# Kernel tuning notes

Measured on AMD Instinct MI355X. Metric: run time of the kernel, lower is better.

Reference implementation:

```python
import jax, jax.numpy as jnp
import numpy as np

D_MODEL = 32
NHEAD = 4
NUM_LAYERS = 4
WINDOW = 256
D_FF = 2 * D_MODEL
INPUT_DIM = 58
MAX_DEPTH = 12
HEAD_OUT = 25


def _layernorm(x, g, b, eps=1e-5):
    m = jnp.mean(x, axis=-1, keepdims=True)
    v = jnp.mean((x - m) ** 2, axis=-1, keepdims=True)
    return (x - m) / jnp.sqrt(v + eps) * g + b


def _layer(h, ipw, ipb, opw, opb, g1, b1, w1, bb1, w2, bb2, g2, b2):
    # Post-norm transformer layer (subclass overrides parent's norm_first path).
    Wn, S, D = h.shape
    dh = D // NHEAD
    qkv = h @ ipw.T + ipb                      # [Wn, S, 3D]
    q, k, v = jnp.split(qkv, 3, axis=-1)
    q = q.reshape(Wn, S, NHEAD, dh).transpose(0, 2, 1, 3)  # [Wn,H,S,dh]
    k = k.reshape(Wn, S, NHEAD, dh).transpose(0, 2, 1, 3)
    v = v.reshape(Wn, S, NHEAD, dh).transpose(0, 2, 1, 3)
    scores = jnp.einsum('whqd,whkd->whqk', q, k) / jnp.sqrt(jnp.asarray(dh, h.dtype))
    a = jax.nn.softmax(scores, axis=-1)        # eager attn weights (need_weights=True path)
    o = jnp.einsum('whqk,whkd->whqd', a, v).transpose(0, 2, 1, 3).reshape(Wn, S, D)
    o = o @ opw.T + opb
    h = _layernorm(h + o, g1, b1)
    ff = jax.nn.gelu(h @ w1.T + bb1, approximate=False) @ w2.T + bb2
    return _layernorm(h + ff, g2, b2)


def setup_inputs() -> dict:
    key = jax.random.key(0)
    ks = jax.random.split(key, 24)
    B, N = 2, 65536
    x = jax.random.uniform(ks[0], (B, N, INPUT_DIM), dtype=jnp.float32)
    layers = jax.random.randint(ks[1], (B, N), 0, MAX_DEPTH)

    def w(k, shape, s=0.05):
        return jax.random.normal(k, shape, jnp.float32) * s

    L = NUM_LAYERS
    return dict(
        x=x,
        layers=layers,
        feature_proj_w=w(ks[2], (D_MODEL, INPUT_DIM)),
        feature_proj_b=w(ks[3], (D_MODEL,)),
        layer_embed=w(ks[4], (MAX_DEPTH, D_MODEL)),
        fourier_B=jax.random.normal(ks[5], (3, D_MODEL // 2), jnp.float32) * 1024.0,
        in_proj_w=w(ks[6], (L, 3 * D_MODEL, D_MODEL)),
        in_proj_b=w(ks[7], (L, 3 * D_MODEL)),
        out_proj_w=w(ks[8], (L, D_MODEL, D_MODEL)),
        out_proj_b=w(ks[9], (L, D_MODEL)),
        ln1_g=jnp.ones((L, D_MODEL), jnp.float32),
        ln1_b=jnp.zeros((L, D_MODEL), jnp.float32),
        lin1_w=w(ks[10], (L, D_FF, D_MODEL)),
        lin1_b=w(ks[11], (L, D_FF)),
        lin2_w=w(ks[12], (L, D_MODEL, D_FF)),
        lin2_b=w(ks[13], (L, D_MODEL)),
        ln2_g=jnp.ones((L, D_MODEL), jnp.float32),
        ln2_b=jnp.zeros((L, D_MODEL), jnp.float32),
        norm_out_g=jnp.ones((D_MODEL,), jnp.float32),
        norm_out_b=jnp.zeros((D_MODEL,), jnp.float32),
        head_w=w(ks[14], (HEAD_OUT, D_MODEL)),
        head_b=w(ks[15], (HEAD_OUT,)),
    )


def reference(x, layers, feature_proj_w, feature_proj_b, layer_embed, fourier_B,
              in_proj_w, in_proj_b, out_proj_w, out_proj_b,
              ln1_g, ln1_b, lin1_w, lin1_b, lin2_w, lin2_b, ln2_g, ln2_b,
              norm_out_g, norm_out_b, head_w, head_b):
    B, N, _ = x.shape
    pos = x[:, :, :3]
    proj = (2.0 * jnp.pi) * (pos @ fourier_B)                  # [B,N,D/2]
    pe = jnp.concatenate([jnp.sin(proj), jnp.cos(proj)], axis=-1)
    h = x @ feature_proj_w.T + feature_proj_b + layer_embed[layers] + pe
    # N chosen divisible by WINDOW, so pad_len == 0 (original pads otherwise)
    nw = N // WINDOW
    h = h.reshape(B * nw, WINDOW, D_MODEL)
    for i in range(NUM_LAYERS):
        h = _layer(h, in_proj_w[i], in_proj_b[i], out_proj_w[i], out_proj_b[i],
                   ln1_g[i], ln1_b[i], lin1_w[i], lin1_b[i], lin2_w[i], lin2_b[i],
                   ln2_g[i], ln2_b[i])
    h = h.reshape(B, N, D_MODEL)
    return _layernorm(h, norm_out_g, norm_out_b) @ head_w.T + head_b
```

## Files before the change

kernel.cpp:

```cpp
#include <hip/hip_runtime.h>

constexpr int S    = 256;
constexpr int D    = 32;
constexpr int NH   = 4;
constexpr int DH   = 8;
constexpr int DFF  = 64;
constexpr int NL   = 4;
constexpr int IND  = 58;
constexpr int HOUT = 25;
constexpr int TPB  = 256;

typedef float  f2 __attribute__((ext_vector_type(2)));
typedef float  f4 __attribute__((ext_vector_type(4)));
typedef __fp16 h2 __attribute__((ext_vector_type(2)));
typedef __fp16 h4 __attribute__((ext_vector_type(4)));
typedef __fp16 h8 __attribute__((ext_vector_type(8)));

__device__ __forceinline__ f4 MFMA16(h4 a, h4 b, f4 c) {
  return __builtin_amdgcn_mfma_f32_16x16x16f16(a, b, c, 0, 0, 0);
}
__device__ __forceinline__ f4 MFMA32(h8 a, h8 b, f4 c) {
  return __builtin_amdgcn_mfma_f32_16x16x32_f16(a, b, c, 0, 0, 0);
}
__device__ __forceinline__ h8 hcat(h4 a, h4 b) {
  return __builtin_shufflevector(a, b, 0, 1, 2, 3, 4, 5, 6, 7);
}

constexpr int HOFF  = 0;
constexpr int QKOFF = 16384;
constexpr int VOFF  = 49152;

__device__ __forceinline__ unsigned pk2(float a, float b) {
  h2 h = __builtin_amdgcn_cvt_pkrtz(a, b);
  return __builtin_bit_cast(unsigned, h);
}

__device__ __forceinline__ float exp2fast(float x) {
#if __has_builtin(__builtin_amdgcn_exp2f)
  return __builtin_amdgcn_exp2f(x);
#else
  return exp2f(x);
#endif
}

__device__ __forceinline__ void wave_fence() {
  __builtin_amdgcn_wave_barrier();
  __builtin_amdgcn_sched_barrier(0);
}

template<int NF2>
__device__ __forceinline__ float dotp(const float* __restrict__ w,
                                      const float* __restrict__ v) {
  const f2* W = (const f2*)w;
  const f2* V = (const f2*)v;
  f2 a0 = {0.f, 0.f}, a1 = {0.f, 0.f};
#pragma unroll
  for (int i = 0; i < NF2; i += 2) a0 += V[i] * W[i];
#pragma unroll
  for (int i = 1; i < NF2; i += 2) a1 += V[i] * W[i];
  f2 s = a0 + a1;
  return s.x + s.y;
}

__device__ __forceinline__ float gelu(float x) {
  float u = 2.3022082f * fmaf(0.044715f * x * x, x, x);
  return x * __builtin_amdgcn_rcpf(1.0f + exp2fast(-u));
}

__device__ __forceinline__ void lnorm(float* h, const float* __restrict__ g,
                                      const float* __restrict__ b) {
  f2* hv = (f2*)h;
  f2 s0 = hv[0], s1 = hv[1];
#pragma unroll
  for (int i = 2; i < 16; i += 2) { s0 += hv[i]; s1 += hv[i + 1]; }
  f2 s = s0 + s1;
  const float m = (s.x + s.y) * (1.0f / D);
  const f2 m2 = {m, m};
  f2 v0 = {0.f, 0.f}, v1 = {0.f, 0.f};
#pragma unroll
  for (int i = 0; i < 16; i += 2) {
    f2 c0 = hv[i] - m2;     v0 += c0 * c0;
    f2 c1 = hv[i + 1] - m2; v1 += c1 * c1;
  }
  f2 vs = v0 + v1;
  const float inv = __builtin_amdgcn_rsqf((vs.x + vs.y) * (1.0f / D) + 1e-5f);
  const f2 inv2 = {inv, inv};
  const f2 mi2 = {-m * inv, -m * inv};
  const f2* g2 = (const f2*)g;
  const f2* b2 = (const f2*)b;
#pragma unroll
  for (int i = 0; i < 16; ++i) {
    f2 t = hv[i] * inv2 + mi2;
    hv[i] = t * g2[i] + b2[i];
  }
}

__device__ __forceinline__ void embed_token(
    const float* __restrict__ xrow, int lay,
    const float* __restrict__ fpw, const float* __restrict__ fpb,
    const float* __restrict__ lemb, const float* __restrict__ fB,
    float* __restrict__ h) {
  float xr[IND];
  const f2* xv = (const f2*)xrow;
#pragma unroll
  for (int i = 0; i < 29; ++i) { f2 t = xv[i]; xr[2 * i] = t.x; xr[2 * i + 1] = t.y; }
  const float* le = lemb + lay * D;
  float pe[D];
#pragma unroll
  for (int k = 0; k < 16; ++k) {
    float t = xr[0] * fB[k] + xr[1] * fB[16 + k] + xr[2] * fB[32 + k];
#if __has_builtin(__builtin_amdgcn_sinf) && __has_builtin(__builtin_amdgcn_cosf) && __has_builtin(__builtin_amdgcn_fractf)
    float u = __builtin_amdgcn_fractf(t);
    pe[k]      = __builtin_amdgcn_sinf(u);
    pe[16 + k] = __builtin_amdgcn_cosf(u);
#else
    float sv, cv;
    sincosf(6.2831853071795864f * (t - floorf(t)), &sv, &cv);
    pe[k] = sv; pe[16 + k] = cv;
#endif
  }
#pragma unroll
  for (int d = 0; d < D; ++d)
    h[d] = dotp<29>(fpw + d * IND, xr) + fpb[d] + le[d] + pe[d];
}

__device__ __forceinline__ h4 bfrag(const float* __restrict__ W, int row,
                                    int K, int kh, int quad) {
  f4 w = *(const f4*)(W + row * K + kh * 16 + quad * 4);
  uint2 p{pk2(w.x, w.y), pk2(w.z, w.w)};
  return __builtin_bit_cast(h4, p);
}
__device__ __forceinline__ h8 bfrag8(const float* __restrict__ W, int row,
                                     int quad) {
  return hcat(bfrag(W, row, 32, 0, quad), bfrag(W, row, 32, 1, quad));
}
__device__ __forceinline__ h4 afrag32(const unsigned char* sm, int base,
                                      int tok, int kh, int quad) {
  return *(const h4*)(sm + base + tok * 64 + (((kh * 4 + quad) ^ (tok & 7)) * 8));
}
__device__ __forceinline__ h8 afrag8(const unsigned char* sm, int base,
                                     int tok, int quad) {
  return hcat(afrag32(sm, base, tok, 0, quad), afrag32(sm, base, tok, 1, quad));
}

__device__ __forceinline__ void store_h16(unsigned char* sm, int tok,
                                          const float* __restrict__ h) {
#pragma unroll
  for (int c = 0; c < 8; ++c) {
    uint2 p{pk2(h[4 * c], h[4 * c + 1]), pk2(h[4 * c + 2], h[4 * c + 3])};
    *(uint2*)(sm + HOFF + tok * 64 + ((c ^ (tok & 7)) * 8)) = p;
  }
}
__device__ __forceinline__ void add_row32(const unsigned char* sm, int base,
                                          int tok, float* __restrict__ h) {
  f2* hv = (f2*)h;
#pragma unroll
  for (int c = 0; c < 8; ++c) {
    h4 q = *(const h4*)(sm + base + tok * 64 + ((c ^ (tok & 7)) * 8));
    f2 lo = {(float)q[0], (float)q[1]};
    f2 hi = {(float)q[2], (float)q[3]};
    hv[2 * c] += lo;
    hv[2 * c + 1] += hi;
  }
}

__global__ void __launch_bounds__(TPB, 2)
spai_fused(const float* __restrict__ x,    const int*   __restrict__ layers,
           const float* __restrict__ fpw,  const float* __restrict__ fpb,
           const float* __restrict__ lemb, const float* __restrict__ fB,
           const float* __restrict__ ipw,  const float* __restrict__ ipb,
           const float* __restrict__ opw,  const float* __restrict__ opb,
           const float* __restrict__ ln1g, const float* __restrict__ ln1b,
           const float* __restrict__ w1,   const float* __restrict__ b1,
           const float* __restrict__ w2,   const float* __restrict__ b2,
           const float* __restrict__ ln2g, const float* __restrict__ ln2b,
           const float* __restrict__ nog,  const float* __restrict__ nob,
           const float* __restrict__ hw,   const float* __restrict__ hb,
           float* __restrict__ out) {
  __shared__ __align__(16) unsigned char sm[65536];
  const int tid  = threadIdx.x;
  const int lane = tid & 63;
  const int wave = tid >> 6;
  const int n16  = lane & 15;
  const int quad = lane >> 4;
  const int qs   = quad & 1;
  const size_t blk_tok = (size_t)blockIdx.x * S;

  float h[D];
  embed_token(x + (blk_tok + tid) * IND, layers[blk_tok + tid],
              fpw, fpb, lemb, fB, h);
  store_h16(sm, tid, h);

  for (int l = 0; l < NL; ++l) {
    __syncthreads();

    const float* Wi = ipw + l * (3 * D) * D;
    const float* Bi = ipb + l * (3 * D);

    {
      h8 Bf[6]; f4 bqk[4]; float bv[2];
#pragma unroll
      for (int nt = 0; nt < 6; ++nt) {
        const float sc = (nt < 2) ? 0.51006973f : 1.0f;
        f4 w0 = *(const f4*)(Wi + (nt * 16 + n16) * D + quad * 4) * sc;
        f4 w1 = *(const f4*)(Wi + (nt * 16 + n16) * D + 16 + quad * 4) * sc;
        uint2 p0{pk2(w0.x, w0.y), pk2(w0.z, w0.w)};
        uint2 p1{pk2(w1.x, w1.y), pk2(w1.z, w1.w)};
        Bf[nt] = hcat(__builtin_bit_cast(h4, p0), __builtin_bit_cast(h4, p1));
        if (nt < 4)
          bqk[nt] = *(const f4*)(Bi + nt * 16 + quad * 4) * sc;
        else
          bv[nt - 4] = Bi[nt * 16 + n16];
      }
      h8 Ah[4];
#pragma unroll
      for (int it = 0; it < 4; ++it)
        Ah[it] = afrag8(sm, HOFF, (wave * 4 + it) * 16 + n16, quad);
      const int kswz = n16 & 7;
#pragma unroll
      for (int it = 0; it < 4; ++it) {
        const int tok = (wave * 4 + it) * 16 + n16;
#pragma unroll
        for (int nt = 0; nt < 4; ++nt) {
          f4 C = MFMA32(Bf[nt], Ah[it], bqk[nt]);
          uint2 p{pk2(C[0], C[1]), pk2(C[2], C[3])};
          *(uint2*)(sm + QKOFF + tok * 128 +
                    (((nt * 2 + (quad >> 1)) ^ kswz) * 16) + (quad & 1) * 8) = p;
        }
#pragma unroll
        for (int nt = 4; nt < 6; ++nt) {
          const float bb = bv[nt - 4];
          f4 C = MFMA32(Ah[it], Bf[nt], (f4){bb, bb, bb, bb});
          uint2 p{pk2(C[0], C[1]), pk2(C[2], C[3])};
          const int vf = (nt - 4) * 16 + n16;
          const int tc = (wave * 4 + it) * 4 + quad;
          *(uint2*)(sm + VOFF + vf * 512 + ((tc ^ ((vf & 7) << 1)) * 8)) = p;
        }
      }
    }
    __syncthreads();

    {
      const int hh  = wave;
      const int m   = n16;
      const int msw = m & 7;
      h4 Kf[16]; h8 Vf8[8];
      const int kbase = QKOFF + (((4 + hh) ^ msw) * 16) + qs * 8;
#pragma unroll
      for (int jt = 0; jt < 16; ++jt) {
        uint2 a = *(const uint2*)(sm + kbase + (jt * 16 + m) * 128);
        if (quad >= 2) { a.x = 0u; a.y = 0u; }
        Kf[jt] = __builtin_bit_cast(h4, a);
      }
      const unsigned fill = (m == 8) ? 0x3C003C00u : 0u;
      const int vbase = VOFF + (hh * 8 + msw) * 512;
      const int vkey  = msw << 1;
#pragma unroll
      for (int j2 = 0; j2 < 8; ++j2) {
        uint2 a = *(const uint2*)(sm + vbase + ((((2 * j2) * 4 + quad) ^ vkey) * 8));
        uint2 b = *(const uint2*)(sm + vbase + ((((2 * j2 + 1) * 4 + quad) ^ vkey) * 8));
        if (m >= 8) { a.x = fill; a.y = fill; b.x = fill; b.y = fill; }
        Vf8[j2] = hcat(__builtin_bit_cast(h4, a), __builtin_bit_cast(h4, b));
      }
      const int qoff = QKOFF + ((hh ^ msw) * 16) + qs * 8;
      const int ooff = HOFF + (((hh * 2 + quad) ^ msw) * 8);

#pragma unroll 2
      for (int it = 0; it < 16; ++it) {
        const int ti = it * 16 + m;
        h4 Qf = *(const h4*)(sm + qoff + ti * 128);
        f4 Of0 = {0.f, 0.f, 0.f, 0.f}, Of1 = {0.f, 0.f, 0.f, 0.f};
        const f4 Z = {0.f, 0.f, 0.f, 0.f};
#pragma unroll
        for (int j2 = 0; j2 < 8; ++j2) {
          f4 T0 = MFMA16(Kf[2 * j2], Qf, Z);
          f4 T1 = MFMA16(Kf[2 * j2 + 1], Qf, Z);
          uint2 pa{pk2(exp2fast(T0[0]), exp2fast(T0[1])),
                   pk2(exp2fast(T0[2]), exp2fast(T0[3]))};
          uint2 pb{pk2(exp2fast(T1[0]), exp2fast(T1[1])),
                   pk2(exp2fast(T1[2]), exp2fast(T1[3]))};
          h8 P8 = hcat(__builtin_bit_cast(h4, pa), __builtin_bit_cast(h4, pb));
          if (j2 & 1) Of1 = MFMA32(Vf8[j2], P8, Of1);
          else        Of0 = MFMA32(Vf8[j2], P8, Of0);
        }
        f4 Of = Of0 + Of1;
        float rinv = __builtin_amdgcn_rcpf(Of[0]);
        rinv = __builtin_bit_cast(
            float, __builtin_amdgcn_ds_bpermute(
                       (32 + m) << 2, __builtin_bit_cast(int, rinv)));
        if (quad < 2) {
          f4 o = Of * rinv;
          uint2 p{pk2(o[0], o[1]), pk2(o[2], o[3])};
          *(uint2*)(sm + ooff + ti * 64) = p;
        }
      }
    }
    __syncthreads();

    {
      const float* Wo = opw + l * D * D;
      const float* Bo = opb + l * D;
      h8 WoF[2]; f4 bo2[2];
#pragma unroll
      for (int nt = 0; nt < 2; ++nt) {
        bo2[nt] = *(const f4*)(Bo + nt * 16 + quad * 4);
        WoF[nt] = bfrag8(Wo, nt * 16 + n16, quad);
      }
      const int kswz = n16 & 7;
#pragma unroll
      for (int ii = 0; ii < 4; ++ii) {
        const int tok = (wave * 4 + ii) * 16 + n16;
        h8 A8 = afrag8(sm, HOFF, tok, quad);
#pragma unroll
        for (int nt = 0; nt < 2; ++nt) {
          f4 C = MFMA32(WoF[nt], A8, bo2[nt]);
          uint2 p{pk2(C[0], C[1]), pk2(C[2], C[3])};
          *(uint2*)(sm + VOFF + tok * 64 + (((nt * 4 + quad) ^ kswz) * 8)) = p;
        }
      }
    }
    wave_fence();

    add_row32(sm, VOFF, tid, h);
    lnorm(h, ln1g + l * D, ln1b + l * D);
    store_h16(sm, tid, h);
    wave_fence();

    {
      const float* Wa = w1 + l * DFF * D;
      const float* Ba = b1 + l * DFF;
      const float* Wb = w2 + l * D * DFF;
      const float* Bb = b2 + l * D;
      h8 WaF[4]; f4 ba4[4]; h8 WbF[4]; f4 bb2[2];
#pragma unroll
      for (int ft = 0; ft < 4; ++ft) {
        ba4[ft] = *(const f4*)(Ba + ft * 16 + quad * 4);
        WaF[ft] = bfrag8(Wa, ft * 16 + n16, quad);
      }
#pragma unroll
      for (int nt = 0; nt < 2; ++nt) {
        bb2[nt] = *(const f4*)(Bb + nt * 16 + quad * 4);
#pragma unroll
        for (int g = 0; g < 2; ++g)
          WbF[nt * 2 + g] = hcat(bfrag(Wb, nt * 16 + n16, 64, 2 * g, quad),
                                 bfrag(Wb, nt * 16 + n16, 64, 2 * g + 1, quad));
      }
      const int kswz = n16 & 7;
#pragma unroll
      for (int tt = 0; tt < 4; ++tt) {
        const int tok = (wave * 4 + tt) * 16 + n16;
        h8 A8 = afrag8(sm, HOFF, tok, quad);
        h4 Pf[4];
#pragma unroll
        for (int ft = 0; ft < 4; ++ft) {
          f4 C = MFMA32(WaF[ft], A8, ba4[ft]);
          uint2 p{pk2(gelu(C[0]), gelu(C[1])), pk2(gelu(C[2]), gelu(C[3]))};
          Pf[ft] = __builtin_bit_cast(h4, p);
        }
        h8 P8a = hcat(Pf[0], Pf[1]);
        h8 P8b = hcat(Pf[2], Pf[3]);
#pragma unroll
        for (int nt = 0; nt < 2; ++nt) {
          f4 C = MFMA32(WbF[nt * 2], P8a, bb2[nt]);
          C = MFMA32(WbF[nt * 2 + 1], P8b, C);
          uint2 p{pk2(C[0], C[1]), pk2(C[2], C[3])};
          *(uint2*)(sm + VOFF + tok * 64 + (((nt * 4 + quad) ^ kswz) * 8)) = p;
        }
      }
    }
    wave_fence();

    add_row32(sm, VOFF, tid, h);
    lnorm(h, ln2g + l * D, ln2b + l * D);
    if (l < NL - 1) store_h16(sm, tid, h);
  }

  __syncthreads();
  lnorm(h, nog, nob);
  float* hs = (float*)sm;
#pragma unroll
  for (int o = 0; o < HOUT; ++o)
    hs[tid * HOUT + o] = dotp<16>(hw + o * D, h) + hb[o];
  __syncthreads();
  f2* og = (f2*)(out + blk_tok * HOUT);
  const f2* os2 = (const f2*)hs;
  for (int i = tid; i < S * HOUT / 2; i += TPB) og[i] = os2[i];
}

extern "C" void kernel_launch(void* const* d_in, const int* in_sizes, int n_in,
                              void* d_out, int out_size, void* d_ws, size_t ws_size,
                              hipStream_t stream) {
  const float* x    = (const float*)d_in[0];
  const int*   lays = (const int*)  d_in[1];
  const float* fpw  = (const float*)d_in[2];
  const float* fpb  = (const float*)d_in[3];
  const float* lemb = (const float*)d_in[4];
  const float* fB   = (const float*)d_in[5];
  const float* ipw  = (const float*)d_in[6];
  const float* ipb  = (const float*)d_in[7];
  const float* opw  = (const float*)d_in[8];
  const float* opb  = (const float*)d_in[9];
  const float* ln1g = (const float*)d_in[10];
  const float* ln1b = (const float*)d_in[11];
  const float* w1   = (const float*)d_in[12];
  const float* b1   = (const float*)d_in[13];
  const float* w2   = (const float*)d_in[14];
  const float* b2   = (const float*)d_in[15];
  const float* ln2g = (const float*)d_in[16];
  const float* ln2b = (const float*)d_in[17];
  const float* nog  = (const float*)d_in[18];
  const float* nob  = (const float*)d_in[19];
  const float* hw   = (const float*)d_in[20];
  const float* hb   = (const float*)d_in[21];
  float* out = (float*)d_out;

  const int nwin = in_sizes[0] / (S * IND);
  spai_fused<<<nwin, TPB, 0, stream>>>(x, lays, fpw, fpb, lemb, fB, ipw, ipb,
                                       opw, opb, ln1g, ln1b, w1, b1, w2, b2,
                                       ln2g, ln2b, nog, nob, hw, hb, out);
}
```

Baseline: 236.7 us.

## Compute per-head QKV projection in registers, drop K/V LDS round trip and a barrier

```diff
diff --git a/kernel.cpp b/kernel.cpp
--- a/kernel.cpp
+++ b/kernel.cpp
@@ -27,8 +27,9 @@
 }
 
 constexpr int HOFF  = 0;
-constexpr int QKOFF = 16384;
-constexpr int VOFF  = 49152;
+constexpr int VOFF  = 16384;
+constexpr int QOFF  = 32768;
+constexpr int LDSSZ = 49152;
 
 __device__ __forceinline__ unsigned pk2(float a, float b) {
   h2 h = __builtin_amdgcn_cvt_pkrtz(a, b);
@@ -133,6 +134,14 @@
 __device__ __forceinline__ h8 bfrag8(const float* __restrict__ W, int row,
                                      int quad) {
   return hcat(bfrag(W, row, 32, 0, quad), bfrag(W, row, 32, 1, quad));
+}
+__device__ __forceinline__ h8 wfrag8(const float* __restrict__ W, int row,
+                                     int quad, float sc) {
+  f4 w0 = *(const f4*)(W + row * D + quad * 4) * sc;
+  f4 w1 = *(const f4*)(W + row * D + 16 + quad * 4) * sc;
+  uint2 p0{pk2(w0.x, w0.y), pk2(w0.z, w0.w)};
+  uint2 p1{pk2(w1.x, w1.y), pk2(w1.z, w1.w)};
+  return hcat(__builtin_bit_cast(h4, p0), __builtin_bit_cast(h4, p1));
 }
 __device__ __forceinline__ h4 afrag32(const unsigned char* sm, int base,
                                       int tok, int kh, int quad) {
@@ -177,13 +186,15 @@
            const float* __restrict__ nog,  const float* __restrict__ nob,
            const float* __restrict__ hw,   const float* __restrict__ hb,
            float* __restrict__ out) {
-  __shared__ __align__(16) unsigned char sm[65536];
-  const int tid  = threadIdx.x;
-  const int lane = tid & 63;
-  const int wave = tid >> 6;
-  const int n16  = lane & 15;
-  const int quad = lane >> 4;
-  const int qs   = quad & 1;
+  __shared__ __align__(16) unsigned char sm[LDSSZ];
+  const int tid    = threadIdx.x;
+  const int lane   = tid & 63;
+  const int wave   = tid >> 6;
+  const int n16    = lane & 15;
+  const int quad   = lane >> 4;
+  const int pairi  = wave >> 1;
+  const int parity = wave & 1;
+  const int qbank  = QOFF + pairi * 8192;
   const size_t blk_tok = (size_t)blockIdx.x * S;
 
   float h[D];
@@ -197,80 +208,55 @@
     const float* Wi = ipw + l * (3 * D) * D;
     const float* Bi = ipb + l * (3 * D);
 
+    h4 Kf[16], Vf[16];
     {
-      h8 Bf[6]; f4 bqk[4]; float bv[2];
-#pragma unroll
-      for (int nt = 0; nt < 6; ++nt) {
-        const float sc = (nt < 2) ? 0.51006973f : 1.0f;
-        f4 w0 = *(const f4*)(Wi + (nt * 16 + n16) * D + quad * 4) * sc;
-        f4 w1 = *(const f4*)(Wi + (nt * 16 + n16) * D + 16 + quad * 4) * sc;
-        uint2 p0{pk2(w0.x, w0.y), pk2(w0.z, w0.w)};
-        uint2 p1{pk2(w1.x, w1.y), pk2(w1.z, w1.w)};
-        Bf[nt] = hcat(__builtin_bit_cast(h4, p0), __builtin_bit_cast(h4, p1));
-        if (nt < 4)
-          bqk[nt] = *(const f4*)(Bi + nt * 16 + quad * 4) * sc;
-        else
-          bv[nt - 4] = Bi[nt * 16 + n16];
-      }
-      h8 Ah[4];
-#pragma unroll
-      for (int it = 0; it < 4; ++it)
-        Ah[it] = afrag8(sm, HOFF, (wave * 4 + it) * 16 + n16, quad);
-      const int kswz = n16 & 7;
-#pragma unroll
-      for (int it = 0; it < 4; ++it) {
-        const int tok = (wave * 4 + it) * 16 + n16;
-#pragma unroll
-        for (int nt = 0; nt < 4; ++nt) {
-          f4 C = MFMA32(Bf[nt], Ah[it], bqk[nt]);
-          uint2 p{pk2(C[0], C[1]), pk2(C[2], C[3])};
-          *(uint2*)(sm + QKOFF + tok * 128 +
-                    (((nt * 2 + (quad >> 1)) ^ kswz) * 16) + (quad & 1) * 8) = p;
-        }
-#pragma unroll
-        for (int nt = 4; nt < 6; ++nt) {
-          const float bb = bv[nt - 4];
-          f4 C = MFMA32(Ah[it], Bf[nt], (f4){bb, bb, bb, bb});
-          uint2 p{pk2(C[0], C[1]), pk2(C[2], C[3])};
-          const int vf = (nt - 4) * 16 + n16;
-          const int tc = (wave * 4 + it) * 4 + quad;
-          *(uint2*)(sm + VOFF + vf * 512 + ((tc ^ ((vf & 7) << 1)) * 8)) = p;
-        }
+      const float scq = 0.51006973f;
+      h8 BfQ = wfrag8(Wi, pairi * 16 + n16, quad, scq);
+      h8 BfK = wfrag8(Wi + 32 * D, pairi * 16 + n16, quad, 1.0f);
+      h8 BfV = wfrag8(Wi + 64 * D, pairi * 16 + n16, quad, 1.0f);
+      f4 bq = *(const f4*)(Bi + pairi * 16 + quad * 4) * scq;
+      f4 bk = *(const f4*)(Bi + 32 + pairi * 16 + quad * 4);
+      const float bvv = Bi[64 + pairi * 16 + n16];
+      const f4 bv4 = {bvv, bvv, bvv, bvv};
+      const unsigned fill = (n16 == 8) ? 0x3C003C00u : 0u;
+      const int qsw = (n16 >> 2) & 3;
+#pragma unroll
+      for (int it = 0; it < 16; ++it) {
+        const int tok = it * 16 + n16;
+        h8 Ah = afrag8(sm, HOFF, tok, quad);
+        f4 Cq = MFMA32(BfQ, Ah, bq);
+        f4 Ck = MFMA32(BfK, Ah, bk);
+        f4 Cv = MFMA32(Ah, BfV, bv4);
+        uint2 q{pk2(Cq[0], Cq[1]), pk2(Cq[2], Cq[3])};
+        *(uint2*)(sm + qbank + tok * 32 + ((quad ^ qsw) * 8)) = q;
+        uint2 kk{pk2(Ck[0], Ck[1]), pk2(Ck[2], Ck[3])};
+        Kf[it] = __builtin_bit_cast(h4, kk);
+        uint2 v{pk2(Cv[0], Cv[1]), pk2(Cv[2], Cv[3])};
+        if (parity) {
+          v.x = (unsigned)__shfl_xor((int)v.x, 8);
+          v.y = (unsigned)__shfl_xor((int)v.y, 8);
+        }
+        if (n16 >= 8) { v.x = fill; v.y = fill; }
+        Vf[it] = __builtin_bit_cast(h4, v);
       }
     }
-    __syncthreads();
+    wave_fence();
 
     {
       const int hh  = wave;
       const int m   = n16;
       const int msw = m & 7;
-      h4 Kf[16]; h8 Vf8[8];
-      const int kbase = QKOFF + (((4 + hh) ^ msw) * 16) + qs * 8;
-#pragma unroll
-      for (int jt = 0; jt < 16; ++jt) {
-        uint2 a = *(const uint2*)(sm + kbase + (jt * 16 + m) * 128);
-        if (quad >= 2) { a.x = 0u; a.y = 0u; }
-        Kf[jt] = __builtin_bit_cast(h4, a);
-      }
-      const unsigned fill = (m == 8) ? 0x3C003C00u : 0u;
-      const int vbase = VOFF + (hh * 8 + msw) * 512;
-      const int vkey  = msw << 1;
-#pragma unroll
-      for (int j2 = 0; j2 < 8; ++j2) {
-        uint2 a = *(const uint2*)(sm + vbase + ((((2 * j2) * 4 + quad) ^ vkey) * 8));
-        uint2 b = *(const uint2*)(sm + vbase + ((((2 * j2 + 1) * 4 + quad) ^ vkey) * 8));
-        if (m >= 8) { a.x = fill; a.y = fill; b.x = fill; b.y = fill; }
-        Vf8[j2] = hcat(__builtin_bit_cast(h4, a), __builtin_bit_cast(h4, b));
-      }
-      const int qoff = QKOFF + ((hh ^ msw) * 16) + qs * 8;
-      const int ooff = HOFF + (((hh * 2 + quad) ^ msw) * 8);
-
+      const int ooff = VOFF + (((hh * 2 + quad) ^ msw) * 8);
+      const int qrd  = qbank + ((quad ^ ((m >> 2) & 3)) * 8);
+      const bool qdead = (quad >> 1) != parity;
+      const f4 Z = {0.f, 0.f, 0.f, 0.f};
 #pragma unroll 2
       for (int it = 0; it < 16; ++it) {
         const int ti = it * 16 + m;
-        h4 Qf = *(const h4*)(sm + qoff + ti * 128);
-        f4 Of0 = {0.f, 0.f, 0.f, 0.f}, Of1 = {0.f, 0.f, 0.f, 0.f};
-        const f4 Z = {0.f, 0.f, 0.f, 0.f};
+        uint2 qv = *(const uint2*)(sm + qrd + ti * 32);
+        if (qdead) { qv.x = 0u; qv.y = 0u; }
+        h4 Qf = __builtin_bit_cast(h4, qv);
+        f4 Of0 = Z, Of1 = Z;
 #pragma unroll
         for (int j2 = 0; j2 < 8; ++j2) {
           f4 T0 = MFMA16(Kf[2 * j2], Qf, Z);
@@ -280,8 +266,9 @@
           uint2 pb{pk2(exp2fast(T1[0]), exp2fast(T1[1])),
                    pk2(exp2fast(T1[2]), exp2fast(T1[3]))};
           h8 P8 = hcat(__builtin_bit_cast(h4, pa), __builtin_bit_cast(h4, pb));
-          if (j2 & 1) Of1 = MFMA32(Vf8[j2], P8, Of1);
-          else        Of0 = MFMA32(Vf8[j2], P8, Of0);
+          h8 V8 = hcat(Vf[2 * j2], Vf[2 * j2 + 1]);
+          if (j2 & 1) Of1 = MFMA32(V8, P8, Of1);
+          else        Of0 = MFMA32(V8, P8, Of0);
         }
         f4 Of = Of0 + Of1;
         float rinv = __builtin_amdgcn_rcpf(Of[0]);
@@ -310,7 +297,7 @@
 #pragma unroll
       for (int ii = 0; ii < 4; ++ii) {
         const int tok = (wave * 4 + ii) * 16 + n16;
-        h8 A8 = afrag8(sm, HOFF, tok, quad);
+        h8 A8 = afrag8(sm, VOFF, tok, quad);
 #pragma unroll
         for (int nt = 0; nt < 2; ++nt) {
           f4 C = MFMA32(WoF[nt], A8, bo2[nt]);
```

New measurement: 239.1 us. About the same (+1.1%).
